# Optimization experiments

Hardware: AMD Instinct MI355X
Metric: run time of the kernel (lower is better)

The kernel has to match this reference:

```python
import jax, jax.numpy as jnp
import numpy as np

REF_GROUND_RES = 0.2  # reference_ground_resolution
PR_MIN = 0.2          # pr_min


def setup_inputs() -> dict:
    key = jax.random.key(0)
    k1, k2, k3, k4 = jax.random.split(key, 4)
    B, H, W, N = 8, 512, 512, 128
    pred_hm = jax.random.normal(k1, (B, 1, H, W), dtype=jnp.float32)
    pred_sm = jax.random.normal(k2, (B, 1, H, W), dtype=jnp.float32)
    # per-sample ground resolution in [0.1, 0.5] (avoid divide-by-zero)
    ground_resolution = jax.random.uniform(k3, (B,), dtype=jnp.float32) * 0.4 + 0.1
    mask = jnp.ones((B, 1, H, W), dtype=jnp.float32)
    centers = jax.random.randint(k4, (B, N, 2), 0, H, dtype=jnp.int32)
    return {"pred_hm": pred_hm, "pred_sm": pred_sm,
            "ground_resolution": ground_resolution, "mask": mask,
            "centers": centers}


def _draw_gaussian_broadcast(H, W, centers_f, sigmas):
    # centers_f: [N,2] float (row, col); sigmas: [N]
    yy = jnp.arange(H, dtype=centers_f.dtype)
    xx = jnp.arange(W, dtype=centers_f.dtype)
    dy2 = (yy[None, :] - centers_f[:, 0:1]) ** 2            # [N,H]
    dx2 = (xx[None, :] - centers_f[:, 1:2]) ** 2            # [N,W]
    d2 = dy2[:, :, None] + dx2[:, None, :]                   # [N,H,W]
    g = jnp.exp(-d2 / (2.0 * (sigmas[:, None, None] ** 2)))  # per-center gaussian
    return jnp.max(g, axis=0)                                 # [H,W] max-splat


def reference(pred_hm, pred_sm, ground_resolution, mask, centers):
    B, _, H, W = pred_hm.shape

    def per_sample(hm, sm, c, gr, m):
        sm0 = sm[0]                                # [H,W]
        scale_loss = jnp.mean(sm0 ** 2)
        c = jnp.clip(c, 0, H - 1)                   # clamp like torch.clamp(..., max=H-1)
        # predicted per-center sigma from scale map at the center locations
        sizes = PR_MIN / gr + jax.nn.relu(sm0[c[:, 0], c[:, 1]]) * REF_GROUND_RES / gr
        gt = _draw_gaussian_broadcast(H, W, c.astype(hm.dtype), sizes)
        hm_loss = jnp.mean((hm[0] - gt) ** 2 * m[0])
        return scale_loss, hm_loss, gt

    sl, hl, gts = jax.vmap(per_sample)(pred_hm, pred_sm, centers,
                                       ground_resolution, mask)
    return jnp.mean(sl), jnp.mean(hl), gts[:, None, :, :]
```

## Files before the change

### kernel.cpp

```cpp
#include <hip/hip_runtime.h>

#define HH 512
#define WW 512
#define NB 8
#define NC 128
#define TW 64
#define TH 64
#define TILES_X (WW / TW)
#define TILES_Y (HH / TH)
#define NTILES (TILES_X * TILES_Y)
#define CUT 30.0f


__global__ __launch_bounds__(256) void ahl_main_kernel(
    const float* __restrict__ pred_hm,
    const float* __restrict__ pred_sm,
    const float* __restrict__ mask,
    const float* __restrict__ ground_res,
    const int*   __restrict__ centers,
    float* __restrict__ out,
    float2* __restrict__ partials) {
    __shared__ float4 sp[NC];
    __shared__ float4 sc[NC];
    __shared__ int s_cnt;
    __shared__ float red[8];

    const int b    = blockIdx.x >> 6;
    const int tile = blockIdx.x & 63;
    const int tx0  = (tile & 7) * TW;
    const int ty0  = (tile >> 3) * TH;
    const int tid  = threadIdx.x;

    if (tid == 0) s_cnt = 0;
    if (tid < NC) {
        int cy = centers[(b * NC + tid) * 2 + 0];
        int cx = centers[(b * NC + tid) * 2 + 1];
        cy = min(max(cy, 0), HH - 1);
        cx = min(max(cx, 0), WW - 1);
        float sm = pred_sm[(size_t)b * HH * WW + (size_t)cy * WW + cx];
        float g  = ground_res[b];
        float size = (0.2f / g) * (1.0f + fmaxf(sm, 0.0f));
        float s = 0.70710678f / size;
        sp[tid] = make_float4(s, -(float)cx * s, -(float)cy * s, 0.0f);
    }
    __syncthreads();

    if (tid < NC) {
        float4 P = sp[tid];
        float a0 = fmaf((float)tx0,            P.x, P.y);
        float a1 = fmaf((float)(tx0 + TW - 1), P.x, P.y);
        float b0 = fmaf((float)ty0,            P.x, P.z);
        float b1 = fmaf((float)(ty0 + TH - 1), P.x, P.z);
        float dx = fmaxf(0.0f, fmaxf(a0, -a1));
        float dy = fmaxf(0.0f, fmaxf(b0, -b1));
        if (fmaf(dx, dx, dy * dy) < CUT) {
            int i = atomicAdd(&s_cnt, 1);
            sc[i] = P;
        }
    }
    __syncthreads();
    const int cnt = s_cnt;

    const float c0f = (float)(tx0 + (tid & 31));
    const float c1f = c0f + 32.0f;
    const int   rb  = ty0 + (tid >> 5);
    float rf[8];
#pragma unroll
    for (int r = 0; r < 8; r++) rf[r] = (float)(rb + r * 8);

    float m0[8], m1[8];
#pragma unroll
    for (int r = 0; r < 8; r++) { m0[r] = 1e30f; m1[r] = 1e30f; }

    for (int i = 0; i < cnt; i++) {
        float4 P = sc[i];
        float dxs0 = fmaf(c0f, P.x, P.y);
        float dxs1 = fmaf(c1f, P.x, P.y);
        float dx20 = dxs0 * dxs0;
        float dx21 = dxs1 * dxs1;
#pragma unroll
        for (int r = 0; r < 8; r++) {
            float dys = fmaf(rf[r], P.x, P.z);
            float a = dys * dys;
            m0[r] = fminf(m0[r], dx20 + a);
            m1[r] = fminf(m1[r], dx21 + a);
        }
    }

    float lhm = 0.0f, lsc = 0.0f;
    const size_t sbase = (size_t)b * HH * WW;
    const int col0 = tx0 + (tid & 31);
#pragma unroll
    for (int r = 0; r < 8; r++) {
        size_t rowbase = sbase + (size_t)(rb + r * 8) * WW;
#pragma unroll
        for (int p = 0; p < 2; p++) {
            size_t idx = rowbase + col0 + p * 32;
            float gt = __expf(-(p == 0 ? m0[r] : m1[r]));
            out[2 + idx] = gt;
            float hm = pred_hm[idx];
            float mk = mask[idx];
            float sm = pred_sm[idx];
            float d = hm - gt;
            lhm = fmaf(d * d, mk, lhm);
            lsc = fmaf(sm, sm, lsc);
        }
    }

#pragma unroll
    for (int off = 32; off > 0; off >>= 1) {
        lhm += __shfl_down(lhm, off);
        lsc += __shfl_down(lsc, off);
    }
    int lane = tid & 63, wid = tid >> 6;
    if (lane == 0) { red[wid] = lsc; red[4 + wid] = lhm; }
    __syncthreads();
    if (tid == 0) {
        float ts = red[0] + red[1] + red[2] + red[3];
        float th = red[4] + red[5] + red[6] + red[7];
        partials[blockIdx.x] = make_float2(ts, th);
    }
}

__global__ __launch_bounds__(256) void ahl_reduce_kernel(
    const float2* __restrict__ partials, float* __restrict__ out) {
    __shared__ float red[8];
    const int tid = threadIdx.x;
    float2 a = partials[tid];
    float2 c = partials[tid + 256];
    float ts = a.x + c.x;
    float th = a.y + c.y;
#pragma unroll
    for (int off = 32; off > 0; off >>= 1) {
        ts += __shfl_down(ts, off);
        th += __shfl_down(th, off);
    }
    int lane = tid & 63, wid = tid >> 6;
    if (lane == 0) { red[wid] = ts; red[4 + wid] = th; }
    __syncthreads();
    if (tid == 0) {
        const float invc = 1.0f / (float)((size_t)NB * HH * WW);
        out[0] = (red[0] + red[1] + red[2] + red[3]) * invc;
        out[1] = (red[4] + red[5] + red[6] + red[7]) * invc;
    }
}

extern "C" void kernel_launch(void* const* d_in, const int* in_sizes, int n_in,
                              void* d_out, int out_size, void* d_ws, size_t ws_size,
                              hipStream_t stream) {
    const float* pred_hm    = (const float*)d_in[0];
    const float* pred_sm    = (const float*)d_in[1];
    const float* ground_res = (const float*)d_in[2];
    const float* mask       = (const float*)d_in[3];
    const int*   centers    = (const int*)d_in[4];
    float* out = (float*)d_out;
    float2* partials = (float2*)d_ws;

    ahl_main_kernel<<<NB * NTILES, 256, 0, stream>>>(pred_hm, pred_sm, mask,
                                                     ground_res, centers, out,
                                                     partials);
    ahl_reduce_kernel<<<1, 256, 0, stream>>>(partials, out);
}
```

Measured before the change: 86.41 us.

## Shrink tiles to 64x16, vectorize loads, prefetch inputs before gaussian loop

Tiles shrink from 64x64 to 64x16, so there are four times as many blocks. Each thread now covers 4 contiguous pixels in one row instead of 16 scattered pixels. Input maps are loaded as float4 at kernel start so the memory latency overlaps the center culling and the min loop. Smaller tiles tighten the per-tile center cull, at the cost of more blocks repeating the per-center setup, and the reduce kernel now loops over more partials.

```diff
diff --git a/kernel.cpp b/kernel.cpp
--- a/kernel.cpp
+++ b/kernel.cpp
@@ -5,10 +5,9 @@
 #define NB 8
 #define NC 128
 #define TW 64
-#define TH 64
-#define TILES_X (WW / TW)
-#define TILES_Y (HH / TH)
-#define NTILES (TILES_X * TILES_Y)
+#define TH 16
+#define NTILES 256
+#define NBLK (NB * NTILES)
 #define CUT 30.0f
 
 
@@ -25,11 +24,22 @@
     __shared__ int s_cnt;
     __shared__ float red[8];
 
-    const int b    = blockIdx.x >> 6;
-    const int tile = blockIdx.x & 63;
+    const int b    = blockIdx.x >> 8;
+    const int tile = blockIdx.x & 255;
     const int tx0  = (tile & 7) * TW;
     const int ty0  = (tile >> 3) * TH;
     const int tid  = threadIdx.x;
+
+    const int cg  = tid & 15;
+    const int row = tid >> 4;
+    const int x0  = tx0 + cg * 4;
+    const int y   = ty0 + row;
+
+    const size_t sbase = (size_t)b * HH * WW;
+    const size_t idx   = sbase + (size_t)y * WW + x0;
+    float4 hm4 = *(const float4*)&pred_hm[idx];
+    float4 sm4 = *(const float4*)&pred_sm[idx];
+    float4 mk4 = *(const float4*)&mask[idx];
 
     if (tid == 0) s_cnt = 0;
     if (tid < NC) {
@@ -37,9 +47,9 @@
         int cx = centers[(b * NC + tid) * 2 + 1];
         cy = min(max(cy, 0), HH - 1);
         cx = min(max(cx, 0), WW - 1);
-        float sm = pred_sm[(size_t)b * HH * WW + (size_t)cy * WW + cx];
-        float g  = ground_res[b];
-        float size = (0.2f / g) * (1.0f + fmaxf(sm, 0.0f));
+        float smv = pred_sm[sbase + (size_t)cy * WW + cx];
+        float g   = ground_res[b];
+        float size = (0.2f / g) * (1.0f + fmaxf(smv, 0.0f));
         float s = 0.70710678f / size;
         sp[tid] = make_float4(s, -(float)cx * s, -(float)cy * s, 0.0f);
     }
@@ -61,51 +71,40 @@
     __syncthreads();
     const int cnt = s_cnt;
 
-    const float c0f = (float)(tx0 + (tid & 31));
-    const float c1f = c0f + 32.0f;
-    const int   rb  = ty0 + (tid >> 5);
-    float rf[8];
+    const float yfv = (float)y;
+    float xf[4];
 #pragma unroll
-    for (int r = 0; r < 8; r++) rf[r] = (float)(rb + r * 8);
-
-    float m0[8], m1[8];
-#pragma unroll
-    for (int r = 0; r < 8; r++) { m0[r] = 1e30f; m1[r] = 1e30f; }
+    for (int j = 0; j < 4; j++) xf[j] = (float)(x0 + j);
+    float m[4] = {1e30f, 1e30f, 1e30f, 1e30f};
 
     for (int i = 0; i < cnt; i++) {
         float4 P = sc[i];
-        float dxs0 = fmaf(c0f, P.x, P.y);
-        float dxs1 = fmaf(c1f, P.x, P.y);
-        float dx20 = dxs0 * dxs0;
-        float dx21 = dxs1 * dxs1;
+        float dys = fmaf(yfv, P.x, P.z);
+        float a = dys * dys;
 #pragma unroll
-        for (int r = 0; r < 8; r++) {
-            float dys = fmaf(rf[r], P.x, P.z);
-            float a = dys * dys;
-            m0[r] = fminf(m0[r], dx20 + a);
-            m1[r] = fminf(m1[r], dx21 + a);
+        for (int j = 0; j < 4; j++) {
+            float d = fmaf(xf[j], P.x, P.y);
+            m[j] = fminf(m[j], fmaf(d, d, a));
         }
     }
 
-    float lhm = 0.0f, lsc = 0.0f;
-    const size_t sbase = (size_t)b * HH * WW;
-    const int col0 = tx0 + (tid & 31);
-#pragma unroll
-    for (int r = 0; r < 8; r++) {
-        size_t rowbase = sbase + (size_t)(rb + r * 8) * WW;
-#pragma unroll
-        for (int p = 0; p < 2; p++) {
-            size_t idx = rowbase + col0 + p * 32;
-            float gt = __expf(-(p == 0 ? m0[r] : m1[r]));
-            out[2 + idx] = gt;
-            float hm = pred_hm[idx];
-            float mk = mask[idx];
-            float sm = pred_sm[idx];
-            float d = hm - gt;
-            lhm = fmaf(d * d, mk, lhm);
-            lsc = fmaf(sm, sm, lsc);
-        }
-    }
+    float g0 = __expf(-m[0]);
+    float g1 = __expf(-m[1]);
+    float g2 = __expf(-m[2]);
+    float g3 = __expf(-m[3]);
+    float2* gp = (float2*)&out[2 + idx];
+    gp[0] = make_float2(g0, g1);
+    gp[1] = make_float2(g2, g3);
+
+    float d0 = hm4.x - g0, d1 = hm4.y - g1, d2 = hm4.z - g2, d3 = hm4.w - g3;
+    float lhm = d0 * d0 * mk4.x;
+    lhm = fmaf(d1 * d1, mk4.y, lhm);
+    lhm = fmaf(d2 * d2, mk4.z, lhm);
+    lhm = fmaf(d3 * d3, mk4.w, lhm);
+    float lsc = sm4.x * sm4.x;
+    lsc = fmaf(sm4.y, sm4.y, lsc);
+    lsc = fmaf(sm4.z, sm4.z, lsc);
+    lsc = fmaf(sm4.w, sm4.w, lsc);
 
 #pragma unroll
     for (int off = 32; off > 0; off >>= 1) {
@@ -126,10 +125,12 @@
     const float2* __restrict__ partials, float* __restrict__ out) {
     __shared__ float red[8];
     const int tid = threadIdx.x;
-    float2 a = partials[tid];
-    float2 c = partials[tid + 256];
-    float ts = a.x + c.x;
-    float th = a.y + c.y;
+    float ts = 0.0f, th = 0.0f;
+    for (int s = tid; s < NBLK; s += 256) {
+        float2 a = partials[s];
+        ts += a.x;
+        th += a.y;
+    }
 #pragma unroll
     for (int off = 32; off > 0; off >>= 1) {
         ts += __shfl_down(ts, off);
@@ -156,8 +157,8 @@
     float* out = (float*)d_out;
     float2* partials = (float2*)d_ws;
 
-    ahl_main_kernel<<<NB * NTILES, 256, 0, stream>>>(pred_hm, pred_sm, mask,
-                                                     ground_res, centers, out,
-                                                     partials);
+    ahl_main_kernel<<<NBLK, 256, 0, stream>>>(pred_hm, pred_sm, mask,
+                                              ground_res, centers, out,
+                                              partials);
     ahl_reduce_kernel<<<1, 256, 0, stream>>>(partials, out);
 }
```

After: 85.34 us. Within noise of the previous version (-1.2%).
